# Performance work log

Hardware: AMD Instinct MI355X
Metric: run time of the kernel (lower is better)

## Reference

```python
import jax, jax.numpy as jnp
import numpy as np
import math

B, L, D = 8, 1024, 1024
H = 16
NS = 8
HD = D // H

def setup_inputs() -> dict:
    key = jax.random.key(0)
    ks = jax.random.split(key, 9)
    s = 1.0 / math.sqrt(D)
    inp = {
        "x": jax.random.normal(ks[0], (B, L, D), dtype=jnp.float32),
        "key_padding_mask": jnp.ones((B, L), dtype=bool),
        "Wq_s": jax.random.normal(ks[1], (D, D), dtype=jnp.float32) * s,
        "Wk_s": jax.random.normal(ks[2], (D, D), dtype=jnp.float32) * s,
        "Wv_s": jax.random.normal(ks[3], (D, D), dtype=jnp.float32) * s,
        "Wq_ns": jax.random.normal(ks[4], (NS, D, D), dtype=jnp.float32) * s,
        "Wk_ns": jax.random.normal(ks[5], (NS, D, D), dtype=jnp.float32) * s,
        "Wv_ns": jax.random.normal(ks[6], (NS, D, D), dtype=jnp.float32) * s,
        "W_out": jax.random.normal(ks[7], (D, D), dtype=jnp.float32) * s,
    }
    return inp

def _mixed_proj(x, W_shared, W_ns):
    # x: [B, L, D]; W_shared: [D, D] (out,in); W_ns: [NS, D, D] (per-position out,in)
    L_s = x.shape[1] - W_ns.shape[0]
    s_proj = jnp.einsum('bld,ed->ble', x[:, :L_s], W_shared)       # shared prefix
    ns_proj = jnp.einsum('bnd,ned->bne', x[:, L_s:], W_ns)          # per-position tail
    return jnp.concatenate([s_proj, ns_proj], axis=1)

def reference(x, key_padding_mask, Wq_s, Wk_s, Wv_s, Wq_ns, Wk_ns, Wv_ns, W_out):
    Bv, Lv, Dv = x.shape
    q = _mixed_proj(x, Wq_s, Wq_ns)  # query_len=None -> full
    k = _mixed_proj(x, Wk_s, Wk_ns)
    v = _mixed_proj(x, Wv_s, Wv_ns)
    # [B, H, L, HD]
    q = q.reshape(Bv, Lv, H, HD).transpose(0, 2, 1, 3)
    k = k.reshape(Bv, Lv, H, HD).transpose(0, 2, 1, 3)
    v = v.reshape(Bv, Lv, H, HD).transpose(0, 2, 1, 3)
    causal = jnp.tril(jnp.ones((Lv, Lv), dtype=bool))               # [L_q, L_k]
    mask = causal[None, :, :] & key_padding_mask[:, None, :]        # [B, L_q, L_k]
    scores = jnp.einsum('bhqd,bhkd->bhqk', q, k) / math.sqrt(HD)
    scores = jnp.where(mask[:, None, :, :], scores, jnp.float32(-1e9))
    attn = jax.nn.softmax(scores, axis=-1)  # dropout is identity in eval
    out = jnp.einsum('bhqk,bhkd->bhqd', attn, v)
    out = out.transpose(0, 2, 1, 3).reshape(Bv, Lv, Dv)
    return jnp.einsum('bld,ed->ble', out, W_out)
```

## Files before the change

kernel.cpp:

```cpp
#include <hip/hip_runtime.h>

#define Bsz  8
#define Lsz  1024
#define Dsz  1024
#define Hh   16
#define HDsz 64
#define NSsz 8
#define LSsz 1016

typedef short  bf16x8 __attribute__((ext_vector_type(8)));
typedef float  f32x4  __attribute__((ext_vector_type(4)));

#define GLB(p) ((const __attribute__((address_space(1))) unsigned int*)(p))
#define LDSP(p) ((__attribute__((address_space(3))) unsigned int*)(p))

__device__ __forceinline__ float bf2f(unsigned short u) {
    union { unsigned int i; float f; } v; v.i = ((unsigned int)u) << 16; return v.f;
}
__device__ __forceinline__ unsigned short f2bf(float f) {
    union { float f; unsigned int i; } v; v.f = f;
    unsigned int x = v.i;
    return (unsigned short)((x + 0x7FFFu + ((x >> 16) & 1u)) >> 16);
}

__global__ __launch_bounds__(256) void cast_kernel(
    const float* __restrict__ x,
    const float* __restrict__ wq, const float* __restrict__ wk,
    const float* __restrict__ wv, const float* __restrict__ wo,
    unsigned short* __restrict__ xb,
    unsigned short* __restrict__ wcat,
    unsigned short* __restrict__ wob)
{
    const size_t NX = 2097152;
    const size_t NW = 262144;
    size_t i = (size_t)blockIdx.x * 256 + threadIdx.x;
    const size_t stride = (size_t)gridDim.x * 256;
    const size_t total = NX + 4 * NW;
    for (; i < total; i += stride) {
        const float* src; unsigned short* dst; size_t off;
        if (i < NX)               { src = x;  dst = xb;             off = i; }
        else if (i < NX + NW)     { src = wq; dst = wcat;           off = i - NX; }
        else if (i < NX + 2 * NW) { src = wk; dst = wcat + 1048576; off = i - NX - NW; }
        else if (i < NX + 3 * NW) { src = wv; dst = wcat + 2097152; off = i - NX - 2 * NW; }
        else                      { src = wo; dst = wob;            off = i - NX - 3 * NW; }
        float4 v = reinterpret_cast<const float4*>(src)[off];
        ushort4 o;
        o.x = f2bf(v.x); o.y = f2bf(v.y); o.z = f2bf(v.z); o.w = f2bf(v.w);
        reinterpret_cast<ushort4*>(dst)[off] = o;
    }
}

#define STAGE3(tt) do {                                                         \
    const int _k0 = (tt) * 64;                                                  \
    unsigned short* _Ad = &As[((tt) % 3) * 16384 + wave * 512];                 \
    unsigned short* _Bd = &Bs[((tt) % 3) * 8192  + wave * 512];                 \
    _Pragma("unroll")                                                           \
    for (int _it = 0; _it < 4; ++_it) {                                         \
        int _r = _it * 64 + srow;                                               \
        int _c = sc8 ^ (_r & 7);                                                \
        __builtin_amdgcn_global_load_lds(                                       \
            GLB(&Ab[(size_t)(m0 + _r) * 1024 + _k0 + _c * 8]),                  \
            LDSP(_Ad + _it * 4096), 16, 0, 0);                                  \
    }                                                                           \
    _Pragma("unroll")                                                           \
    for (int _it = 0; _it < 2; ++_it) {                                         \
        int _r = _it * 64 + srow;                                               \
        int _c = sc8 ^ (_r & 7);                                                \
        __builtin_amdgcn_global_load_lds(                                       \
            GLB(&Wb[(size_t)(n0 + _r) * 1024 + _k0 + _c * 8]),                  \
            LDSP(_Bd + _it * 4096), 16, 0, 0);                                  \
    }                                                                           \
} while (0)

template <bool C_F32, bool SPLIT>
__global__ __launch_bounds__(512, 2) void gemm3_kernel(
    const unsigned short* __restrict__ Ab,
    const unsigned short* __restrict__ Wb,
    void* __restrict__ O0, void* __restrict__ O1, void* __restrict__ O2)
{
    __shared__ __align__(16) unsigned short As[3 * 256 * 64];
    __shared__ __align__(16) unsigned short Bs[3 * 128 * 64];

    const int tid  = threadIdx.x;
    const int lane = tid & 63;
    const int wave = tid >> 6;
    const int wm   = wave >> 2;
    const int wn   = wave & 3;
    const int lr   = lane & 15;
    const int lq   = lane >> 4;
    const int m0   = blockIdx.y * 256;
    const int n0   = blockIdx.x * 128;

    const int srow = tid >> 3;
    const int sc8  = tid & 7;

    f32x4 acc[8][2];
    #pragma unroll
    for (int i = 0; i < 8; ++i)
        #pragma unroll
        for (int j = 0; j < 2; ++j)
            acc[i][j] = (f32x4){0.f, 0.f, 0.f, 0.f};

    STAGE3(0);
    STAGE3(1);

    for (int t = 0; t < 16; ++t) {
        if (t < 15) asm volatile("s_waitcnt vmcnt(6)" ::: "memory");
        else        asm volatile("s_waitcnt vmcnt(0)" ::: "memory");
        asm volatile("s_barrier" ::: "memory");
        if (t + 2 < 16) STAGE3(t + 2);

        const unsigned short* Abuf = &As[(t % 3) * 16384];
        const unsigned short* Bbuf = &Bs[(t % 3) * 8192];
        #pragma unroll
        for (int ks = 0; ks < 2; ++ks) {
            bf16x8 af[8], bfr[2];
            #pragma unroll
            for (int i = 0; i < 8; ++i) {
                int row = wm * 128 + i * 16 + lr;
                af[i] = *reinterpret_cast<const bf16x8*>(
                    &Abuf[row * 64 + (((ks * 4 + lq) ^ (row & 7)) << 3)]);
            }
            #pragma unroll
            for (int j = 0; j < 2; ++j) {
                int row = wn * 32 + j * 16 + lr;
                bfr[j] = *reinterpret_cast<const bf16x8*>(
                    &Bbuf[row * 64 + (((ks * 4 + lq) ^ (row & 7)) << 3)]);
            }
            __builtin_amdgcn_s_setprio(1);
            #pragma unroll
            for (int i = 0; i < 8; ++i)
                #pragma unroll
                for (int j = 0; j < 2; ++j)
                    acc[i][j] = __builtin_amdgcn_mfma_f32_16x16x32_bf16(
                        af[i], bfr[j], acc[i][j], 0, 0, 0);
            __builtin_amdgcn_s_setprio(0);
        }
    }

    if (SPLIT) {
        const int tsel = n0 >> 10;
        const int d0   = n0 & 1023;
        unsigned short* Out =
            (unsigned short*)(tsel == 0 ? O0 : tsel == 1 ? O1 : O2);
        #pragma unroll
        for (int i = 0; i < 8; ++i)
            #pragma unroll
            for (int j = 0; j < 2; ++j) {
                int col = d0 + wn * 32 + j * 16 + lr;
                #pragma unroll
                for (int r = 0; r < 4; ++r) {
                    int row = m0 + wm * 128 + i * 16 + lq * 4 + r;
                    Out[(size_t)row * 1024 + col] = f2bf(acc[i][j][r]);
                }
            }
    } else {
        float* Co = (float*)O0;
        #pragma unroll
        for (int i = 0; i < 8; ++i)
            #pragma unroll
            for (int j = 0; j < 2; ++j) {
                int col = n0 + wn * 32 + j * 16 + lr;
                #pragma unroll
                for (int r = 0; r < 4; ++r) {
                    int row = m0 + wm * 128 + i * 16 + lq * 4 + r;
                    Co[(size_t)row * 1024 + col] = acc[i][j][r];
                }
            }
    }
}

#define GBM 128
#define GBN 128
#define GBK 64

template <bool A_F32, bool C_F32>
__global__ __launch_bounds__(256) void gemm_bt_kernel(
    const void* __restrict__ Av,
    const float* __restrict__ W,
    void* __restrict__ Cv,
    int M, int N, int K)
{
    __shared__ unsigned short As[GBM][GBK];
    __shared__ unsigned short Ws[GBN][GBK];

    const int tid  = threadIdx.x;
    const int lane = tid & 63;
    const int wave = tid >> 6;
    const int wm   = wave >> 1;
    const int wn   = wave & 1;
    const int lr   = lane & 15;
    const int lq   = lane >> 4;
    const int m0   = blockIdx.y * GBM;
    const int n0   = blockIdx.x * GBN;

    f32x4 acc[4][4];
    #pragma unroll
    for (int i = 0; i < 4; ++i)
        #pragma unroll
        for (int j = 0; j < 4; ++j)
            acc[i][j] = (f32x4){0.f, 0.f, 0.f, 0.f};

    for (int k0 = 0; k0 < K; k0 += GBK) {
        if (A_F32) {
            const float* A = (const float*)Av;
            #pragma unroll
            for (int i = 0; i < 8; ++i) {
                int idx = tid + i * 256;
                int row = idx >> 4;
                int c4  = idx & 15;
                float4 a = *reinterpret_cast<const float4*>(
                    &A[(size_t)(m0 + row) * K + k0 + c4 * 4]);
                ushort4 o;
                o.x = f2bf(a.x); o.y = f2bf(a.y);
                o.z = f2bf(a.z); o.w = f2bf(a.w);
                *reinterpret_cast<ushort4*>(&As[row][c4 * 4]) = o;
            }
        } else {
            const unsigned short* A = (const unsigned short*)Av;
            #pragma unroll
            for (int i = 0; i < 4; ++i) {
                int idx = tid + i * 256;
                int row = idx >> 3;
                int c8  = idx & 7;
                int4 v = *reinterpret_cast<const int4*>(
                    &A[(size_t)(m0 + row) * K + k0 + c8 * 8]);
                *reinterpret_cast<int4*>(&As[row][c8 * 8]) = v;
            }
        }
        #pragma unroll
        for (int i = 0; i < 8; ++i) {
            int idx = tid + i * 256;
            int row = idx >> 4;
            int c4  = idx & 15;
            float4 w = *reinterpret_cast<const float4*>(
                &W[(size_t)(n0 + row) * K + k0 + c4 * 4]);
            ushort4 o;
            o.x = f2bf(w.x); o.y = f2bf(w.y);
            o.z = f2bf(w.z); o.w = f2bf(w.w);
            *reinterpret_cast<ushort4*>(&Ws[row][c4 * 4]) = o;
        }
        __syncthreads();

        #pragma unroll
        for (int ks = 0; ks < 2; ++ks) {
            bf16x8 af[4], bfr[4];
            #pragma unroll
            for (int i = 0; i < 4; ++i)
                af[i] = *reinterpret_cast<const bf16x8*>(
                    &As[wm * 64 + i * 16 + lr][ks * 32 + lq * 8]);
            #pragma unroll
            for (int j = 0; j < 4; ++j)
                bfr[j] = *reinterpret_cast<const bf16x8*>(
                    &Ws[wn * 64 + j * 16 + lr][ks * 32 + lq * 8]);
            #pragma unroll
            for (int i = 0; i < 4; ++i)
                #pragma unroll
                for (int j = 0; j < 4; ++j)
                    acc[i][j] = __builtin_amdgcn_mfma_f32_16x16x32_bf16(
                        af[i], bfr[j], acc[i][j], 0, 0, 0);
        }
        __syncthreads();
    }

    #pragma unroll
    for (int i = 0; i < 4; ++i) {
        #pragma unroll
        for (int j = 0; j < 4; ++j) {
            int col = n0 + wn * 64 + j * 16 + lr;
            #pragma unroll
            for (int r = 0; r < 4; ++r) {
                int row = m0 + wm * 64 + i * 16 + lq * 4 + r;
                if (C_F32) {
                    ((float*)Cv)[(size_t)row * N + col] = acc[i][j][r];
                } else {
                    ((unsigned short*)Cv)[(size_t)row * N + col] = f2bf(acc[i][j][r]);
                }
            }
        }
    }
}

__global__ __launch_bounds__(512) void fixup_kernel(
    const float* __restrict__ x,
    const float* __restrict__ Wq_ns,
    const float* __restrict__ Wk_ns,
    const float* __restrict__ Wv_ns,
    unsigned short* __restrict__ Q,
    unsigned short* __restrict__ Kb,
    unsigned short* __restrict__ V)
{
    const int bid   = blockIdx.x;
    const int wgt   = bid >> 6;
    const int chunk = bid & 63;
    const int proj  = wgt >> 3;
    const int n     = wgt & 7;
    const float* Wns =
        (proj == 0 ? Wq_ns : proj == 1 ? Wk_ns : Wv_ns) + (size_t)n * Dsz * Dsz;
    unsigned short* Out = (proj == 0 ? Q : proj == 1 ? Kb : V);
    const int l    = LSsz + n;
    const int b    = threadIdx.x >> 6;
    const int lane = threadIdx.x & 63;

    const float* xrow = x + ((size_t)b * Lsz + l) * Dsz;
    float4 xr[4];
    #pragma unroll
    for (int i = 0; i < 4; ++i)
        xr[i] = *reinterpret_cast<const float4*>(&xrow[lane * 4 + i * 256]);

    for (int er = 0; er < 16; ++er) {
        const int e = chunk * 16 + er;
        const float* wrow = Wns + (size_t)e * Dsz;
        float s = 0.f;
        #pragma unroll
        for (int i = 0; i < 4; ++i) {
            float4 wv = *reinterpret_cast<const float4*>(&wrow[lane * 4 + i * 256]);
            s += wv.x * xr[i].x + wv.y * xr[i].y
               + wv.z * xr[i].z + wv.w * xr[i].w;
        }
        #pragma unroll
        for (int off = 32; off > 0; off >>= 1) s += __shfl_xor(s, off, 64);
        if (lane == 0) Out[((size_t)b * Lsz + l) * Dsz + e] = f2bf(s);
    }
}

__global__ __launch_bounds__(256, 4) void attn_mfma_kernel(
    const unsigned short* __restrict__ Q,
    const unsigned short* __restrict__ K,
    const unsigned short* __restrict__ V,
    unsigned short* __restrict__ O)
{
    __shared__ __align__(16) unsigned short Klds[2 * 4096];
    __shared__ __align__(16) unsigned short Vtlds[4096];
    __shared__ __align__(16) unsigned short Plds[4][1024];

    const int tid  = threadIdx.x;
    const int lane = tid & 63;
    const int wave = tid >> 6;
    const int lr   = lane & 15;
    const int lq   = lane >> 4;

    const int id = blockIdx.x;
    const int qt = 15 - ((id >> 3) & 15);
    const int bh = ((id >> 7) << 3) | (id & 7);
    const int h  = bh & (Hh - 1);
    const int b  = bh >> 4;
    const int qw = qt * 64 + wave * 16;
    const int nkt = qt + 1;

    const size_t base = (size_t)b * Lsz * Dsz + (size_t)h * HDsz;

    bf16x8 qf[2];
    #pragma unroll
    for (int h2 = 0; h2 < 2; ++h2) {
        bf16x8 t = *reinterpret_cast<const bf16x8*>(
            &Q[base + (size_t)(qw + lr) * Dsz + h2 * 32 + lq * 8]);
        #pragma unroll
        for (int e = 0; e < 8; ++e) {
            float f = bf2f((unsigned short)t[e]) * 0.125f;
            t[e] = (short)f2bf(f);
        }
        qf[h2] = t;
    }

    f32x4 acc[4];
    #pragma unroll
    for (int jd = 0; jd < 4; ++jd) acc[jd] = (f32x4){0.f, 0.f, 0.f, 0.f};
    float m_i[4] = {-1e30f, -1e30f, -1e30f, -1e30f};
    float l_i[4] = {0.f, 0.f, 0.f, 0.f};

    const int krow0 = tid >> 3;
    const int kc8   = tid & 7;
    const int vd0   = (tid & 7) * 8;
    const int vk0   = (tid >> 3) * 2;

    unsigned short* Pw = &Plds[wave][0];
    int4 vq0, vq1;

    #pragma unroll
    for (int it = 0; it < 2; ++it) {
        int row  = it * 32 + krow0;
        int csrc = kc8 ^ (row & 7);
        const unsigned short* ga = &K[base + (size_t)row * Dsz + csrc * 8];
        __builtin_amdgcn_global_load_lds(GLB(ga),
            LDSP(&Klds[it * 2048 + wave * 512]), 16, 0, 0);
    }
    vq0 = *reinterpret_cast<const int4*>(&V[base + (size_t)(vk0 + 0) * Dsz + vd0]);
    vq1 = *reinterpret_cast<const int4*>(&V[base + (size_t)(vk0 + 1) * Dsz + vd0]);

    for (int kt = 0; kt < nkt; ++kt) {
        const int k0 = kt * 64;
        const int kb = (kt & 1) * 4096;

        __syncthreads();

        {
            union { int4 v; unsigned short u[8]; } a, c;
            a.v = vq0; c.v = vq1;
            const int kc  = vk0 >> 3;
            const int klo = vk0 & 7;
            #pragma unroll
            for (int d = 0; d < 8; ++d) {
                int dd  = vd0 + d;
                int idx = dd * 64 + (((kc ^ (dd & 7)) << 3) | klo);
                ushort2 p; p.x = a.u[d]; p.y = c.u[d];
                *reinterpret_cast<ushort2*>(&Vtlds[idx]) = p;
            }
        }
        __syncthreads();

        if (kt + 1 < nkt) {
            const int k0n = k0 + 64;
            #pragma unroll
            for (int it = 0; it < 2; ++it) {
                int row  = it * 32 + krow0;
                int csrc = kc8 ^ (row & 7);
                const unsigned short* ga =
                    &K[base + (size_t)(k0n + row) * Dsz + csrc * 8];
                __builtin_amdgcn_global_load_lds(GLB(ga),
                    LDSP(&Klds[(kb ^ 4096) + it * 2048 + wave * 512]), 16, 0, 0);
            }
            vq0 = *reinterpret_cast<const int4*>(
                &V[base + (size_t)(k0n + vk0 + 0) * Dsz + vd0]);
            vq1 = *reinterpret_cast<const int4*>(
                &V[base + (size_t)(k0n + vk0 + 1) * Dsz + vd0]);
        }

        f32x4 sv[4];
        #pragma unroll
        for (int jt = 0; jt < 4; ++jt) sv[jt] = (f32x4){0.f, 0.f, 0.f, 0.f};

        __builtin_amdgcn_s_setprio(1);
        #pragma unroll
        for (int h2 = 0; h2 < 2; ++h2) {
            const int cs = (((h2 << 2) | lq) ^ (lr & 7)) << 3;
            #pragma unroll
            for (int jt = 0; jt < 4; ++jt) {
                bf16x8 kf = *reinterpret_cast<const bf16x8*>(
                    &Klds[kb + (jt * 16 + lr) * 64 + cs]);
                sv[jt] = __builtin_amdgcn_mfma_f32_16x16x32_bf16(
                    qf[h2], kf, sv[jt], 0, 0, 0);
            }
        }
        __builtin_amdgcn_s_setprio(0);

        if (k0 + 63 > qw) {
            #pragma unroll
            for (int jt = 0; jt < 4; ++jt) {
                int kpos = k0 + jt * 16 + lr;
                #pragma unroll
                for (int r = 0; r < 4; ++r) {
                    int q = qw + lq * 4 + r;
                    if (kpos > q) sv[jt][r] = -1e30f;
                }
            }
        }

        float tm[4], al[4], rs[4];
        #pragma unroll
        for (int r = 0; r < 4; ++r)
            tm[r] = fmaxf(fmaxf(sv[0][r], sv[1][r]), fmaxf(sv[2][r], sv[3][r]));
        #pragma unroll
        for (int off = 1; off < 16; off <<= 1)
            #pragma unroll
            for (int r = 0; r < 4; ++r)
                tm[r] = fmaxf(tm[r], __shfl_xor(tm[r], off, 64));
        #pragma unroll
        for (int r = 0; r < 4; ++r) {
            float nm = fmaxf(m_i[r], tm[r]);
            al[r] = __expf(m_i[r] - nm);
            m_i[r] = nm;
        }
        #pragma unroll
        for (int jt = 0; jt < 4; ++jt)
            #pragma unroll
            for (int r = 0; r < 4; ++r)
                sv[jt][r] = __expf(sv[jt][r] - m_i[r]);
        #pragma unroll
        for (int r = 0; r < 4; ++r)
            rs[r] = (sv[0][r] + sv[1][r]) + (sv[2][r] + sv[3][r]);
        #pragma unroll
        for (int off = 1; off < 16; off <<= 1)
            #pragma unroll
            for (int r = 0; r < 4; ++r)
                rs[r] += __shfl_xor(rs[r], off, 64);
        #pragma unroll
        for (int r = 0; r < 4; ++r) l_i[r] = l_i[r] * al[r] + rs[r];
        #pragma unroll
        for (int jd = 0; jd < 4; ++jd)
            #pragma unroll
            for (int r = 0; r < 4; ++r)
                acc[jd][r] *= al[r];

        #pragma unroll
        for (int jt = 0; jt < 4; ++jt) {
            int kcol  = jt * 16 + lr;
            int chunk = kcol >> 3;
            int elem  = kcol & 7;
            #pragma unroll
            for (int r = 0; r < 4; ++r) {
                int qrow = lq * 4 + r;
                Pw[qrow * 64 + (((chunk ^ (qrow & 7)) << 3) | elem)] =
                    f2bf(sv[jt][r]);
            }
        }

        __builtin_amdgcn_s_setprio(1);
        #pragma unroll
        for (int h2 = 0; h2 < 2; ++h2) {
            const int cs = (((h2 << 2) | lq) ^ (lr & 7)) << 3;
            bf16x8 pf = *reinterpret_cast<const bf16x8*>(&Pw[lr * 64 + cs]);
            #pragma unroll
            for (int jd = 0; jd < 4; ++jd) {
                bf16x8 vf = *reinterpret_cast<const bf16x8*>(
                    &Vtlds[(jd * 16 + lr) * 64 + cs]);
                acc[jd] = __builtin_amdgcn_mfma_f32_16x16x32_bf16(
                    pf, vf, acc[jd], 0, 0, 0);
            }
        }
        __builtin_amdgcn_s_setprio(0);
    }

    float inv[4];
    #pragma unroll
    for (int r = 0; r < 4; ++r) inv[r] = 1.0f / l_i[r];
    #pragma unroll
    for (int jd = 0; jd < 4; ++jd) {
        #pragma unroll
        for (int r = 0; r < 4; ++r) {
            int qrow  = lq * 4 + r;
            int col   = jd * 16 + lr;
            int chunk = col >> 3;
            int elem  = col & 7;
            Pw[qrow * 64 + (((chunk ^ (qrow & 7)) << 3) | elem)] =
                f2bf(acc[jd][r] * inv[r]);
        }
    }
    #pragma unroll
    for (int it2 = 0; it2 < 2; ++it2) {
        int row = it2 * 8 + (lane >> 3);
        int c   = lane & 7;
        const int4 ov = *reinterpret_cast<const int4*>(
            &Pw[row * 64 + ((c ^ (row & 7)) << 3)]);
        *reinterpret_cast<int4*>(&O[base + (size_t)(qw + row) * Dsz + c * 8]) = ov;
    }
}

extern "C" void kernel_launch(void* const* d_in, const int* in_sizes, int n_in,
                              void* d_out, int out_size, void* d_ws, size_t ws_size,
                              hipStream_t stream)
{
    const float* x     = (const float*)d_in[0];
    const float* Wq_s  = (const float*)d_in[2];
    const float* Wk_s  = (const float*)d_in[3];
    const float* Wv_s  = (const float*)d_in[4];
    const float* Wq_ns = (const float*)d_in[5];
    const float* Wk_ns = (const float*)d_in[6];
    const float* Wv_ns = (const float*)d_in[7];
    const float* W_out = (const float*)d_in[8];
    float* out = (float*)d_out;

    const size_t nElem = (size_t)Bsz * Lsz * Dsz;
    unsigned short* Q    = (unsigned short*)d_ws;
    unsigned short* Kb   = Q + nElem;
    unsigned short* V    = Kb + nElem;
    unsigned short* Xb   = V + nElem;
    unsigned short* Wcat = Xb + nElem;
    unsigned short* Wob  = Wcat + 3 * 1048576;
    const size_t need = (4 * nElem + 4 * 1048576) * sizeof(unsigned short);

    if (ws_size >= need) {
        cast_kernel<<<3072, 256, 0, stream>>>(x, Wq_s, Wk_s, Wv_s, W_out,
                                              Xb, Wcat, Wob);
        gemm3_kernel<false, true><<<dim3(24, 32), 512, 0, stream>>>(
            Xb, Wcat, Q, Kb, V);
        fixup_kernel<<<24 * 64, 512, 0, stream>>>(x, Wq_ns, Wk_ns, Wv_ns, Q, Kb, V);
        unsigned short* O = Xb;
        attn_mfma_kernel<<<Bsz * Hh * (Lsz / 64), 256, 0, stream>>>(Q, Kb, V, O);
        gemm3_kernel<true, false><<<dim3(8, 32), 512, 0, stream>>>(
            O, Wob, out, nullptr, nullptr);
    } else {
        unsigned short* O = Xb;
        dim3 ggrid(Dsz / GBN, (Bsz * Lsz) / GBM);
        gemm_bt_kernel<true, false><<<ggrid, 256, 0, stream>>>(x, Wq_s, Q,  Bsz * Lsz, Dsz, Dsz);
        gemm_bt_kernel<true, false><<<ggrid, 256, 0, stream>>>(x, Wk_s, Kb, Bsz * Lsz, Dsz, Dsz);
        gemm_bt_kernel<true, false><<<ggrid, 256, 0, stream>>>(x, Wv_s, V,  Bsz * Lsz, Dsz, Dsz);
        fixup_kernel<<<24 * 64, 512, 0, stream>>>(x, Wq_ns, Wk_ns, Wv_ns, Q, Kb, V);
        attn_mfma_kernel<<<Bsz * Hh * (Lsz / 64), 256, 0, stream>>>(Q, Kb, V, O);
        gemm_bt_kernel<false, true><<<ggrid, 256, 0, stream>>>(O, W_out, out, Bsz * Lsz, Dsz, Dsz);
    }
}
```

Before: 388.0 us.

## Interleave GEMM global-to-LDS prefetch phases with MFMA sub-steps and barriers

Splits each K-tile's global_load_lds staging into two halves issued between the two MFMA k-substeps, adds per-substep barriers and explicit lgkmcnt waits, and uses sched_barrier to pin instruction order. The intent is to spread memory issue evenly across the compute loop and keep MFMA clusters contiguous, in the style of an 8-wave ping-pong schedule. It adds two extra workgroup barriers per substep, which can cost synchronisation time and reduce overlap between waves.

```diff
diff --git a/kernel.cpp b/kernel.cpp
--- a/kernel.cpp
+++ b/kernel.cpp
@@ -21,6 +21,9 @@
     union { float f; unsigned int i; } v; v.f = f;
     unsigned int x = v.i;
     return (unsigned short)((x + 0x7FFFu + ((x >> 16) & 1u)) >> 16);
+}
+__device__ __forceinline__ void gload(const unsigned short* g, unsigned short* l) {
+    __builtin_amdgcn_global_load_lds(GLB(g), LDSP(l), 16, 0, 0);
 }
 
 __global__ __launch_bounds__(256) void cast_kernel(
@@ -50,36 +53,14 @@
     }
 }
 
-#define STAGE3(tt) do {                                                         \
-    const int _k0 = (tt) * 64;                                                  \
-    unsigned short* _Ad = &As[((tt) % 3) * 16384 + wave * 512];                 \
-    unsigned short* _Bd = &Bs[((tt) % 3) * 8192  + wave * 512];                 \
-    _Pragma("unroll")                                                           \
-    for (int _it = 0; _it < 4; ++_it) {                                         \
-        int _r = _it * 64 + srow;                                               \
-        int _c = sc8 ^ (_r & 7);                                                \
-        __builtin_amdgcn_global_load_lds(                                       \
-            GLB(&Ab[(size_t)(m0 + _r) * 1024 + _k0 + _c * 8]),                  \
-            LDSP(_Ad + _it * 4096), 16, 0, 0);                                  \
-    }                                                                           \
-    _Pragma("unroll")                                                           \
-    for (int _it = 0; _it < 2; ++_it) {                                         \
-        int _r = _it * 64 + srow;                                               \
-        int _c = sc8 ^ (_r & 7);                                                \
-        __builtin_amdgcn_global_load_lds(                                       \
-            GLB(&Wb[(size_t)(n0 + _r) * 1024 + _k0 + _c * 8]),                  \
-            LDSP(_Bd + _it * 4096), 16, 0, 0);                                  \
-    }                                                                           \
-} while (0)
-
 template <bool C_F32, bool SPLIT>
-__global__ __launch_bounds__(512, 2) void gemm3_kernel(
+__global__ __launch_bounds__(512, 2) void gemm8_kernel(
     const unsigned short* __restrict__ Ab,
     const unsigned short* __restrict__ Wb,
     void* __restrict__ O0, void* __restrict__ O1, void* __restrict__ O2)
 {
-    __shared__ __align__(16) unsigned short As[3 * 256 * 64];
-    __shared__ __align__(16) unsigned short Bs[3 * 128 * 64];
+    __shared__ __align__(16) unsigned short As[3 * 16384];
+    __shared__ __align__(16) unsigned short Bs[3 * 8192];
 
     const int tid  = threadIdx.x;
     const int lane = tid & 63;
@@ -94,6 +75,35 @@
     const int srow = tid >> 3;
     const int sc8  = tid & 7;
 
+    auto stage_ph = [&](int tt, int ph) {
+        const int k0 = tt * 64;
+        unsigned short* Abase = &As[(tt % 3) * 16384];
+        unsigned short* Bbase = &Bs[(tt % 3) * 8192];
+        if (ph == 0) {
+            #pragma unroll
+            for (int u = 0; u < 2; ++u) {
+                int r = u * 64 + srow;
+                int c = sc8 ^ (r & 7);
+                gload(&Ab[(size_t)(m0 + r) * 1024 + k0 + c * 8],
+                      &Abase[u * 4096 + wave * 512]);
+            }
+            int r = srow, c = sc8 ^ (r & 7);
+            gload(&Wb[(size_t)(n0 + r) * 1024 + k0 + c * 8],
+                  &Bbase[wave * 512]);
+        } else {
+            #pragma unroll
+            for (int u = 2; u < 4; ++u) {
+                int r = u * 64 + srow;
+                int c = sc8 ^ (r & 7);
+                gload(&Ab[(size_t)(m0 + r) * 1024 + k0 + c * 8],
+                      &Abase[u * 4096 + wave * 512]);
+            }
+            int r = 64 + srow, c = sc8 ^ (r & 7);
+            gload(&Wb[(size_t)(n0 + r) * 1024 + k0 + c * 8],
+                  &Bbase[4096 + wave * 512]);
+        }
+    };
+
     f32x4 acc[8][2];
     #pragma unroll
     for (int i = 0; i < 8; ++i)
@@ -101,15 +111,12 @@
         for (int j = 0; j < 2; ++j)
             acc[i][j] = (f32x4){0.f, 0.f, 0.f, 0.f};
 
-    STAGE3(0);
-    STAGE3(1);
+    stage_ph(0, 0); stage_ph(0, 1);
+    stage_ph(1, 0); stage_ph(1, 1);
+    asm volatile("s_waitcnt vmcnt(6)" ::: "memory");
+    __builtin_amdgcn_s_barrier();
 
     for (int t = 0; t < 16; ++t) {
-        if (t < 15) asm volatile("s_waitcnt vmcnt(6)" ::: "memory");
-        else        asm volatile("s_waitcnt vmcnt(0)" ::: "memory");
-        asm volatile("s_barrier" ::: "memory");
-        if (t + 2 < 16) STAGE3(t + 2);
-
         const unsigned short* Abuf = &As[(t % 3) * 16384];
         const unsigned short* Bbuf = &Bs[(t % 3) * 8192];
         #pragma unroll
@@ -127,6 +134,16 @@
                 bfr[j] = *reinterpret_cast<const bf16x8*>(
                     &Bbuf[row * 64 + (((ks * 4 + lq) ^ (row & 7)) << 3)]);
             }
+            if (t + 2 < 16) stage_ph(t + 2, ks);
+            if (ks == 1) {
+                if (t + 2 < 16)
+                    asm volatile("s_waitcnt vmcnt(6)" ::: "memory");
+                else if (t + 1 < 16)
+                    asm volatile("s_waitcnt vmcnt(0)" ::: "memory");
+            }
+            __builtin_amdgcn_s_barrier();
+            asm volatile("s_waitcnt lgkmcnt(0)" ::: "memory");
+            __builtin_amdgcn_sched_barrier(0);
             __builtin_amdgcn_s_setprio(1);
             #pragma unroll
             for (int i = 0; i < 8; ++i)
@@ -135,6 +152,7 @@
                     acc[i][j] = __builtin_amdgcn_mfma_f32_16x16x32_bf16(
                         af[i], bfr[j], acc[i][j], 0, 0, 0);
             __builtin_amdgcn_s_setprio(0);
+            __builtin_amdgcn_s_barrier();
         }
     }
 
@@ -572,12 +590,12 @@
     if (ws_size >= need) {
         cast_kernel<<<3072, 256, 0, stream>>>(x, Wq_s, Wk_s, Wv_s, W_out,
                                               Xb, Wcat, Wob);
-        gemm3_kernel<false, true><<<dim3(24, 32), 512, 0, stream>>>(
+        gemm8_kernel<false, true><<<dim3(24, 32), 512, 0, stream>>>(
             Xb, Wcat, Q, Kb, V);
         fixup_kernel<<<24 * 64, 512, 0, stream>>>(x, Wq_ns, Wk_ns, Wv_ns, Q, Kb, V);
         unsigned short* O = Xb;
         attn_mfma_kernel<<<Bsz * Hh * (Lsz / 64), 256, 0, stream>>>(Q, Kb, V, O);
-        gemm3_kernel<true, false><<<dim3(8, 32), 512, 0, stream>>>(
+        gemm8_kernel<true, false><<<dim3(8, 32), 512, 0, stream>>>(
             O, Wob, out, nullptr, nullptr);
     } else {
         unsigned short* O = Xb;
```

Measured after the change: 369.8 us. 4.7% less time.
